# Optimization experiments

Hardware: AMD Instinct MI355X
Metric: run time of the kernel (lower is better)

The kernel has to match this reference:

```python
import jax, jax.numpy as jnp
import numpy as np

B, S, J, D = 256, 512, 32, 3
LOG_2PI = float(np.log(2.0 * np.pi))


def setup_inputs() -> dict:
    key = jax.random.key(0)
    k1, k2, k3, k4 = jax.random.split(key, 4)
    y_true = jax.random.normal(k1, (B, S, J, D), dtype=jnp.float32)
    y_pred_mean = jax.random.normal(k2, (B, S, J, D), dtype=jnp.float32)
    # Lower-triangular Cholesky factor with strictly positive diagonal.
    L = jnp.tril(jax.random.uniform(k3, (B, S, J, D, D), dtype=jnp.float32))
    diag = jax.random.uniform(k4, (B, S, J, D), dtype=jnp.float32, minval=0.5, maxval=1.5)
    idx = jnp.arange(D)
    L = L.at[..., idx, idx].set(diag)
    return {"y_true": y_true, "y_pred_mean": y_pred_mean, "pred_cholesky_L": L}


def reference(y_true, y_pred_mean, pred_cholesky_L):
    L = pred_cholesky_L
    # log det Sigma = 2 * sum(log(diag(L)))  -- shape (B,S,J)
    diag = jnp.diagonal(L, axis1=-2, axis2=-1)
    log_det_sigma = 2.0 * jnp.sum(jnp.log(diag), axis=-1)
    # Closed-form forward substitution for the 3x3 lower-triangular solve L x = d
    d = y_true - y_pred_mean
    x0 = d[..., 0] / L[..., 0, 0]
    x1 = (d[..., 1] - L[..., 1, 0] * x0) / L[..., 1, 1]
    x2 = (d[..., 2] - L[..., 2, 0] * x0 - L[..., 2, 1] * x1) / L[..., 2, 2]
    mahalanobis = x0 * x0 + x1 * x1 + x2 * x2  # (B,S,J)
    loss = 0.5 * (mahalanobis + log_det_sigma + D * LOG_2PI)
    return jnp.mean(loss)
```

## Files before the change

### kernel.cpp

```cpp
#include <hip/hip_runtime.h>
#include <math.h>

constexpr int NGROUPS = 256 * 512 * 32;
constexpr int NQUAD   = NGROUPS / 4;
constexpr int BLOCK   = 256;
constexpr int GRID    = NQUAD / BLOCK;

#define LOG_2PI 1.8378770664093453f

typedef float f32x4 __attribute__((ext_vector_type(4)));

__device__ __forceinline__ float fast_rcp(float x) {
    return __builtin_amdgcn_rcpf(x);
}

__global__ __launch_bounds__(BLOCK) void nll_main(
    const float* __restrict__ yt,
    const float* __restrict__ yp,
    const float* __restrict__ Lm,
    float* __restrict__ partial)
{
    const f32x4* yt4 = reinterpret_cast<const f32x4*>(yt);
    const f32x4* yp4 = reinterpret_cast<const f32x4*>(yp);
    const f32x4* L4  = reinterpret_cast<const f32x4*>(Lm);

    const int q = blockIdx.x * BLOCK + threadIdx.x;

    float d[12];
    #pragma unroll
    for (int i = 0; i < 3; ++i) {
        f32x4 a = yt4[q * 3 + i];
        f32x4 b = yp4[q * 3 + i];
        d[i * 4 + 0] = a.x - b.x;
        d[i * 4 + 1] = a.y - b.y;
        d[i * 4 + 2] = a.z - b.z;
        d[i * 4 + 3] = a.w - b.w;
    }
    float l[36];
    #pragma unroll
    for (int i = 0; i < 9; ++i) {
        f32x4 v = L4[q * 9 + i];
        l[i * 4 + 0] = v.x;
        l[i * 4 + 1] = v.y;
        l[i * 4 + 2] = v.z;
        l[i * 4 + 3] = v.w;
    }

    float acc = 0.0f;
    #pragma unroll
    for (int g = 0; g < 4; ++g) {
        float L00 = l[g * 9 + 0];
        float L10 = l[g * 9 + 3];
        float L11 = l[g * 9 + 4];
        float L20 = l[g * 9 + 6];
        float L21 = l[g * 9 + 7];
        float L22 = l[g * 9 + 8];
        float d0 = d[g * 3 + 0];
        float d1 = d[g * 3 + 1];
        float d2 = d[g * 3 + 2];

        float r0 = fast_rcp(L00);
        float r1 = fast_rcp(L11);
        float r2 = fast_rcp(L22);
        float x0 = d0 * r0;
        float x1 = (d1 - L10 * x0) * r1;
        float x2 = (d2 - L20 * x0 - L21 * x1) * r2;
        float maha   = x0 * x0 + x1 * x1 + x2 * x2;
        float logdet = __logf(L00) + __logf(L11) + __logf(L22);
        acc += 0.5f * maha + logdet;
    }

    #pragma unroll
    for (int off = 32; off > 0; off >>= 1) acc += __shfl_down(acc, off, 64);

    __shared__ float sdata[BLOCK / 64];
    const int lane = threadIdx.x & 63;
    const int wid  = threadIdx.x >> 6;
    if (lane == 0) sdata[wid] = acc;
    __syncthreads();
    if (threadIdx.x == 0) {
        float s = 0.0f;
        #pragma unroll
        for (int w = 0; w < BLOCK / 64; ++w) s += sdata[w];
        partial[blockIdx.x] = s;
    }
}

__global__ __launch_bounds__(256) void nll_reduce(
    const float* __restrict__ partial, float* __restrict__ out)
{
    float acc = 0.0f;
    for (int i = threadIdx.x; i < GRID; i += 256) acc += partial[i];

    #pragma unroll
    for (int off = 32; off > 0; off >>= 1) acc += __shfl_down(acc, off, 64);

    __shared__ float sdata[4];
    const int lane = threadIdx.x & 63;
    const int wid  = threadIdx.x >> 6;
    if (lane == 0) sdata[wid] = acc;
    __syncthreads();
    if (threadIdx.x == 0) {
        out[0] = (sdata[0] + sdata[1] + sdata[2] + sdata[3]) *
                     (1.0f / (float)NGROUPS) +
                 0.5f * 3.0f * LOG_2PI;
    }
}

extern "C" void kernel_launch(void* const* d_in, const int* in_sizes, int n_in,
                              void* d_out, int out_size, void* d_ws, size_t ws_size,
                              hipStream_t stream)
{
    const float* yt = (const float*)d_in[0];
    const float* yp = (const float*)d_in[1];
    const float* Lm = (const float*)d_in[2];
    float* out      = (float*)d_out;
    float* partial  = (float*)d_ws;

    nll_main<<<GRID, BLOCK, 0, stream>>>(yt, yp, Lm, partial);
    nll_reduce<<<1, 256, 0, stream>>>(partial, out);
}
```

Before: 45.96 us.

## Stage inputs through LDS with coalesced loads, one group per thread

Each thread now handles one group instead of four. Each block first loads its slice of y_true, y_pred and L into shared memory using contiguous vector loads, then reads the scattered fields from LDS. This replaces the strided per-thread vector loads, which left consecutive lanes far apart in memory, and it increases the number of blocks. The final reduce becomes a 1024-thread kernel reading the now larger partial array as float4. The cost is an extra barrier and LDS traffic per block, plus LDS bank conflicts from stride-3 and stride-9 reads.

```diff
diff --git a/kernel.cpp b/kernel.cpp
--- a/kernel.cpp
+++ b/kernel.cpp
@@ -2,9 +2,8 @@
 #include <math.h>
 
 constexpr int NGROUPS = 256 * 512 * 32;
-constexpr int NQUAD   = NGROUPS / 4;
 constexpr int BLOCK   = 256;
-constexpr int GRID    = NQUAD / BLOCK;
+constexpr int GRID    = NGROUPS / BLOCK;
 
 #define LOG_2PI 1.8378770664093453f
 
@@ -20,60 +19,79 @@
     const float* __restrict__ Lm,
     float* __restrict__ partial)
 {
+    __shared__ float syt[768];
+    __shared__ float syp[768];
+    __shared__ float sl[2304];
+
     const f32x4* yt4 = reinterpret_cast<const f32x4*>(yt);
     const f32x4* yp4 = reinterpret_cast<const f32x4*>(yp);
     const f32x4* L4  = reinterpret_cast<const f32x4*>(Lm);
+    f32x4* syt4 = reinterpret_cast<f32x4*>(syt);
+    f32x4* syp4 = reinterpret_cast<f32x4*>(syp);
+    f32x4* sl4  = reinterpret_cast<f32x4*>(sl);
 
-    const int q = blockIdx.x * BLOCK + threadIdx.x;
+    const int tid = threadIdx.x;
+    const int bx  = blockIdx.x;
 
-    float d[12];
+    if (tid < 192) {
+        syt4[tid] = yt4[bx * 192 + tid];
+        syp4[tid] = yp4[bx * 192 + tid];
+    }
+    sl4[tid]       = L4[bx * 576 + tid];
+    sl4[tid + 256] = L4[bx * 576 + 256 + tid];
+    if (tid < 64) sl4[tid + 512] = L4[bx * 576 + 512 + tid];
+    __syncthreads();
+
+    const float d0 = syt[tid * 3 + 0] - syp[tid * 3 + 0];
+    const float d1 = syt[tid * 3 + 1] - syp[tid * 3 + 1];
+    const float d2 = syt[tid * 3 + 2] - syp[tid * 3 + 2];
+    const float L00 = sl[tid * 9 + 0];
+    const float L10 = sl[tid * 9 + 3];
+    const float L11 = sl[tid * 9 + 4];
+    const float L20 = sl[tid * 9 + 6];
+    const float L21 = sl[tid * 9 + 7];
+    const float L22 = sl[tid * 9 + 8];
+
+    const float r0 = fast_rcp(L00);
+    const float r1 = fast_rcp(L11);
+    const float r2 = fast_rcp(L22);
+    const float x0 = d0 * r0;
+    const float x1 = (d1 - L10 * x0) * r1;
+    const float x2 = (d2 - L20 * x0 - L21 * x1) * r2;
+    const float maha = x0 * x0 + x1 * x1 + x2 * x2;
+    float acc = 0.5f * maha + __logf(L00) + __logf(L11) + __logf(L22);
+
     #pragma unroll
-    for (int i = 0; i < 3; ++i) {
-        f32x4 a = yt4[q * 3 + i];
-        f32x4 b = yp4[q * 3 + i];
-        d[i * 4 + 0] = a.x - b.x;
-        d[i * 4 + 1] = a.y - b.y;
-        d[i * 4 + 2] = a.z - b.z;
-        d[i * 4 + 3] = a.w - b.w;
+    for (int off = 32; off > 0; off >>= 1) acc += __shfl_down(acc, off, 64);
+
+    __shared__ float sdata[BLOCK / 64];
+    const int lane = tid & 63;
+    const int wid  = tid >> 6;
+    if (lane == 0) sdata[wid] = acc;
+    __syncthreads();
+    if (tid == 0) {
+        float s = 0.0f;
+        #pragma unroll
+        for (int w = 0; w < BLOCK / 64; ++w) s += sdata[w];
+        partial[bx] = s;
     }
-    float l[36];
-    #pragma unroll
-    for (int i = 0; i < 9; ++i) {
-        f32x4 v = L4[q * 9 + i];
-        l[i * 4 + 0] = v.x;
-        l[i * 4 + 1] = v.y;
-        l[i * 4 + 2] = v.z;
-        l[i * 4 + 3] = v.w;
-    }
+}
 
+__global__ __launch_bounds__(1024) void nll_reduce(
+    const float* __restrict__ partial, float* __restrict__ out)
+{
+    const f32x4* p4 = reinterpret_cast<const f32x4*>(partial);
     float acc = 0.0f;
     #pragma unroll
-    for (int g = 0; g < 4; ++g) {
-        float L00 = l[g * 9 + 0];
-        float L10 = l[g * 9 + 3];
-        float L11 = l[g * 9 + 4];
-        float L20 = l[g * 9 + 6];
-        float L21 = l[g * 9 + 7];
-        float L22 = l[g * 9 + 8];
-        float d0 = d[g * 3 + 0];
-        float d1 = d[g * 3 + 1];
-        float d2 = d[g * 3 + 2];
-
-        float r0 = fast_rcp(L00);
-        float r1 = fast_rcp(L11);
-        float r2 = fast_rcp(L22);
-        float x0 = d0 * r0;
-        float x1 = (d1 - L10 * x0) * r1;
-        float x2 = (d2 - L20 * x0 - L21 * x1) * r2;
-        float maha   = x0 * x0 + x1 * x1 + x2 * x2;
-        float logdet = __logf(L00) + __logf(L11) + __logf(L22);
-        acc += 0.5f * maha + logdet;
+    for (int k = 0; k < 4; ++k) {
+        f32x4 v = p4[threadIdx.x + k * 1024];
+        acc += v.x + v.y + v.z + v.w;
     }
 
     #pragma unroll
     for (int off = 32; off > 0; off >>= 1) acc += __shfl_down(acc, off, 64);
 
-    __shared__ float sdata[BLOCK / 64];
+    __shared__ float sdata[16];
     const int lane = threadIdx.x & 63;
     const int wid  = threadIdx.x >> 6;
     if (lane == 0) sdata[wid] = acc;
@@ -81,29 +99,8 @@
     if (threadIdx.x == 0) {
         float s = 0.0f;
         #pragma unroll
-        for (int w = 0; w < BLOCK / 64; ++w) s += sdata[w];
-        partial[blockIdx.x] = s;
-    }
-}
-
-__global__ __launch_bounds__(256) void nll_reduce(
-    const float* __restrict__ partial, float* __restrict__ out)
-{
-    float acc = 0.0f;
-    for (int i = threadIdx.x; i < GRID; i += 256) acc += partial[i];
-
-    #pragma unroll
-    for (int off = 32; off > 0; off >>= 1) acc += __shfl_down(acc, off, 64);
-
-    __shared__ float sdata[4];
-    const int lane = threadIdx.x & 63;
-    const int wid  = threadIdx.x >> 6;
-    if (lane == 0) sdata[wid] = acc;
-    __syncthreads();
-    if (threadIdx.x == 0) {
-        out[0] = (sdata[0] + sdata[1] + sdata[2] + sdata[3]) *
-                     (1.0f / (float)NGROUPS) +
-                 0.5f * 3.0f * LOG_2PI;
+        for (int w = 0; w < 16; ++w) s += sdata[w];
+        out[0] = s * (1.0f / (float)NGROUPS) + 0.5f * 3.0f * LOG_2PI;
     }
 }
 
@@ -118,5 +115,5 @@
     float* partial  = (float*)d_ws;
 
     nll_main<<<GRID, BLOCK, 0, stream>>>(yt, yp, Lm, partial);
-    nll_reduce<<<1, 256, 0, stream>>>(partial, out);
+    nll_reduce<<<1, 1024, 0, stream>>>(partial, out);
 }
```

Measured after the change: 43.72 us (median of 2 runs). -4.9%, faster.
